# Performance work log

Hardware: AMD Instinct MI355X
Metric: run time of the kernel (lower is better)

The kernel has to match this reference:

```python
import jax, jax.numpy as jnp
import numpy as np

N, E = 50000, 1600000
F_IN, EDGE_DIM, HID, HEADS, NCLS = 64, 16, 128, 4, 40
C = HID // HEADS  # per-head dim = 32


def setup_inputs() -> dict:
    key = jax.random.key(0)
    ks = jax.random.split(key, 20)
    s = 0.1
    inp = {
        'x': jax.random.normal(ks[0], (N, F_IN), jnp.float32),
        'edge_index': jax.random.randint(ks[1], (2, E), 0, N, jnp.int64),
        'edge_attr': jax.random.normal(ks[2], (E, EDGE_DIM), jnp.float32),
        # layer 1 params
        'W1': jax.random.normal(ks[3], (HID, F_IN), jnp.float32) * s,
        'as1': jax.random.normal(ks[4], (HEADS, C), jnp.float32) * s,
        'ad1': jax.random.normal(ks[5], (HEADS, C), jnp.float32) * s,
        'ae1': jax.random.normal(ks[6], (HEADS, C), jnp.float32) * s,
        'We1': jax.random.normal(ks[7], (HID, EDGE_DIM), jnp.float32) * s,
        'b1': jnp.zeros((HID,), jnp.float32),
        # layer 2 params
        'W2': jax.random.normal(ks[8], (HID, HID), jnp.float32) * s,
        'as2': jax.random.normal(ks[9], (HEADS, C), jnp.float32) * s,
        'ad2': jax.random.normal(ks[10], (HEADS, C), jnp.float32) * s,
        'ae2': jax.random.normal(ks[11], (HEADS, C), jnp.float32) * s,
        'We2': jax.random.normal(ks[12], (HID, EDGE_DIM), jnp.float32) * s,
        'b2': jnp.zeros((HID,), jnp.float32),
        # final classifier
        'Wlin': jax.random.normal(ks[13], (NCLS, HID), jnp.float32) * s,
        'blin': jnp.zeros((NCLS,), jnp.float32),
    }
    return inp


def gat_conv(x, src, dst, eattr, W, a_s, a_d, a_e, We, b):
    """PyG GATConv (concat=True, add_self_loops=True, fill_value='mean'), eval mode."""
    n = x.shape[0]
    H, Cd = a_s.shape
    h = (x @ W.T).reshape(n, H, Cd)  # [N,H,C]
    # self-loop edge_attr = per-destination mean of incoming edge_attr
    cnt = jax.ops.segment_sum(jnp.ones((dst.shape[0],), eattr.dtype), dst, num_segments=n)
    mean_ea = jax.ops.segment_sum(eattr, dst, num_segments=n) / jnp.maximum(cnt, 1.0)[:, None]
    loops = jnp.arange(n, dtype=src.dtype)
    s_idx = jnp.concatenate([src, loops])
    d_idx = jnp.concatenate([dst, loops])
    ea = jnp.concatenate([eattr, mean_ea], axis=0)  # [E+N, edge_dim]
    e = (ea @ We.T).reshape(-1, H, Cd)
    # edge-wise attention logits
    alpha = (h * a_s).sum(-1)[s_idx] + (h * a_d).sum(-1)[d_idx] + (e * a_e).sum(-1)  # [E+N,H]
    alpha = jax.nn.leaky_relu(alpha, 0.2)
    # segment softmax over destination neighborhoods (every node has a self-loop)
    amax = jax.ops.segment_max(alpha, d_idx, num_segments=n)
    ex = jnp.exp(alpha - amax[d_idx])
    den = jax.ops.segment_sum(ex, d_idx, num_segments=n)
    coef = ex / (den[d_idx] + 1e-16)
    out = jax.ops.segment_sum(h[s_idx] * coef[:, :, None], d_idx, num_segments=n)
    return out.reshape(n, H * Cd) + b


def reference(x, edge_index, edge_attr, W1, as1, ad1, ae1, We1, b1,
              W2, as2, ad2, ae2, We2, b2, Wlin, blin):
    src, dst = edge_index[0], edge_index[1]
    h = jax.nn.relu(gat_conv(x, src, dst, edge_attr, W1, as1, ad1, ae1, We1, b1))
    h = jax.nn.relu(gat_conv(h, src, dst, edge_attr, W2, as2, ad2, ae2, We2, b2))
    logits = h @ Wlin.T + blin
    return jax.nn.log_softmax(logits, axis=1)
```

## Files before the change

### kernel.cpp

```cpp
#include <hip/hip_runtime.h>
#include <hip/hip_bf16.h>
#include <math.h>


#define CHUNK 2048

typedef __attribute__((ext_vector_type(8))) short short8;
typedef __attribute__((ext_vector_type(4))) float floatx4;
typedef __attribute__((ext_vector_type(2))) float floatx2;

__device__ __forceinline__ unsigned short f2bf(float f) {
  unsigned u = __float_as_uint(f);
  unsigned r = u + 0x7FFFu + ((u >> 16) & 1u);
  return (unsigned short)(r >> 16);
}
__device__ __forceinline__ float bf2f(unsigned short b) {
  return __uint_as_float(((unsigned)b) << 16);
}

__global__ __launch_bounds__(256) void alphaseq_kernel(const float* __restrict__ ea,
                                                       const float* __restrict__ ae1,
                                                       const float* __restrict__ We1,
                                                       const float* __restrict__ ae2,
                                                       const float* __restrict__ We2,
                                                       const int* __restrict__ dst,
                                                       int* __restrict__ bucketCnt,
                                                       uint2* __restrict__ tA1,
                                                       uint2* __restrict__ tA2,
                                                       int E, int NB) {
  __shared__ float wa[128];
  __shared__ int hist[512];
  const int tid = threadIdx.x;
  hist[tid] = 0;
  hist[tid + 256] = 0;
  if (tid < 128) {
    const float* aev = (tid < 64) ? ae1 : ae2;
    const float* Wev = (tid < 64) ? We1 : We2;
    const int h = (tid >> 4) & 3;
    const int d = tid & 15;
    float s = 0.f;
#pragma unroll
    for (int c = 0; c < 32; ++c) s += aev[h * 32 + c] * Wev[(h * 32 + c) * 16 + d];
    wa[tid] = s;
  }
  __syncthreads();
  const int e0 = blockIdx.x * CHUNK, e1 = min(e0 + CHUNK, E);
  for (int e = e0 + tid; e < e1; e += 256) {
    atomicAdd(&hist[dst[e] >> 7], 1);
    const float4* p = (const float4*)(ea + (size_t)e * 16);
    float4 q0 = p[0], q1 = p[1], q2 = p[2], q3 = p[3];
    float v[16] = {q0.x, q0.y, q0.z, q0.w, q1.x, q1.y, q1.z, q1.w,
                   q2.x, q2.y, q2.z, q2.w, q3.x, q3.y, q3.z, q3.w};
    unsigned short rr[8];
#pragma unroll
    for (int h = 0; h < 8; ++h) {
      float s = 0.f;
#pragma unroll
      for (int d = 0; d < 16; ++d) s += v[d] * wa[h * 16 + d];
      rr[h] = f2bf(s);
    }
    uint2 lo, hi;
    lo.x = ((unsigned)rr[1] << 16) | rr[0];
    lo.y = ((unsigned)rr[3] << 16) | rr[2];
    hi.x = ((unsigned)rr[5] << 16) | rr[4];
    hi.y = ((unsigned)rr[7] << 16) | rr[6];
    tA1[e] = lo;
    tA2[e] = hi;
  }
  __syncthreads();
  for (int i = tid; i < NB; i += 256)
    if (hist[i]) atomicAdd(&bucketCnt[i], hist[i]);
}

__global__ __launch_bounds__(512) void scanB_kernel(const int* __restrict__ bucketCnt,
                                                    int* __restrict__ bucketOffs,
                                                    int* __restrict__ bucketPos,
                                                    int* __restrict__ offs,
                                                    int NB, int N, int E) {
  __shared__ int sc[512];
  const int tid = threadIdx.x;
  const int v = (tid < NB) ? bucketCnt[tid] : 0;
  sc[tid] = v;
  __syncthreads();
  for (int off = 1; off < 512; off <<= 1) {
    int t = (tid >= off) ? sc[tid - off] : 0;
    __syncthreads();
    sc[tid] += t;
    __syncthreads();
  }
  const int excl = sc[tid] - v;
  if (tid < NB) { bucketOffs[tid] = excl; bucketPos[tid] = excl; }
  if (tid == 0) { bucketOffs[NB] = E; offs[N] = E; }
}

__global__ __launch_bounds__(512) void partB_kernel(const int* __restrict__ src,
                                                    const int* __restrict__ dst,
                                                    const uint2* __restrict__ tA1,
                                                    const uint2* __restrict__ tA2,
                                                    int* __restrict__ bucketPos,
                                                    int4* __restrict__ binned16,
                                                    int* __restrict__ binned4,
                                                    unsigned char* __restrict__ dlArr,
                                                    int E, int NB) {
  __shared__ int hist[512], gbase[512], lcnt[512];
  const int tid = threadIdx.x;
  const int e0 = blockIdx.x * CHUNK;
  const int e1 = min(e0 + CHUNK, E);
  hist[tid] = 0; lcnt[tid] = 0;
  __syncthreads();
  for (int e = e0 + tid; e < e1; e += 512) atomicAdd(&hist[dst[e] >> 7], 1);
  __syncthreads();
  if (tid < NB && hist[tid] > 0) gbase[tid] = atomicAdd(&bucketPos[tid], hist[tid]);
  __syncthreads();
  for (int e = e0 + tid; e < e1; e += 512) {
    const int d = dst[e];
    const int b = d >> 7;
    const int lr = atomicAdd(&lcnt[b], 1);
    const int g = gbase[b] + lr;
    const uint2 a1 = tA1[e];
    const uint2 a2 = tA2[e];
    int4 v;
    v.x = (src[e] & 0xFFFF) | ((d & 127) << 16);
    v.y = (int)a1.x;
    v.z = (int)a1.y;
    v.w = (int)a2.x;
    binned16[g] = v;
    binned4[g] = (int)a2.y;
    dlArr[g] = (unsigned char)(d & 127);
  }
}

__global__ __launch_bounds__(256) void passC_kernel(const int4* __restrict__ binned16,
                                                    const int* __restrict__ binned4,
                                                    const unsigned char* __restrict__ dlArr,
                                                    const int* __restrict__ bucketOffs,
                                                    int* __restrict__ srcS,
                                                    uint2* __restrict__ aeS1,
                                                    uint2* __restrict__ aeS2,
                                                    int* __restrict__ offs, int N) {
  __shared__ int cnt[128], dbase[129], dpos[128];
  const int tid = threadIdx.x;
  const int b = blockIdx.x;
  const int bo = bucketOffs[b], be = bucketOffs[b + 1];
  const int m = be - bo;
  if (tid < 128) { cnt[tid] = 0; dpos[tid] = 0; }
  __syncthreads();
  for (int t = tid; t < m; t += 256) atomicAdd(&cnt[dlArr[bo + t]], 1);
  __syncthreads();
  for (int off = 1; off < 128; off <<= 1) {
    int t = (tid < 128 && tid >= (unsigned)off) ? cnt[tid - off] : 0;
    __syncthreads();
    if (tid < 128) cnt[tid] += t;
    __syncthreads();
  }
  if (tid == 0) dbase[0] = 0;
  if (tid < 128) dbase[tid + 1] = cnt[tid];
  __syncthreads();
  const int dcnt = min(128, N - (b << 7));
  if (tid < dcnt) offs[(b << 7) + tid] = bo + dbase[tid];
  for (int t = tid; t < m; t += 256) {
    const int4 v = binned16[bo + t];
    const int w4 = binned4[bo + t];
    const int dl = (v.x >> 16) & 127;
    const int p = dbase[dl] + atomicAdd(&dpos[dl], 1);
    srcS[bo + p] = v.x & 0xFFFF;
    aeS1[bo + p] = make_uint2((unsigned)v.y, (unsigned)v.z);
    aeS2[bo + p] = make_uint2((unsigned)v.w, (unsigned)w4);
  }
}

__global__ __launch_bounds__(256) void cvtall_kernel(const float* __restrict__ W1,
                                                     unsigned short* __restrict__ Wb1,
                                                     const float* __restrict__ W2,
                                                     unsigned short* __restrict__ Wb2,
                                                     const float* __restrict__ Wlin,
                                                     unsigned short* __restrict__ whi,
                                                     unsigned short* __restrict__ wlo) {
  const int n1 = 128 * 64, n2 = 128 * 128, n3 = 48 * 128;
  int i = blockIdx.x * 256 + threadIdx.x;
  if (i < n1) {
    Wb1[i] = f2bf(W1[i]);
  } else if (i < n1 + n2) {
    Wb2[i - n1] = f2bf(W2[i - n1]);
  } else if (i < n1 + n2 + n3) {
    const int j = i - n1 - n2;
    float v = (j < 40 * 128) ? Wlin[j] : 0.f;
    unsigned short h = f2bf(v);
    whi[j] = h;
    wlo[j] = f2bf(v - bf2f(h));
  }
}

#define GEMM_SCORE_EPILOGUE()                                                      \
  {                                                                                \
    const float as0 = a_s[ncol0], as1v = a_s[ncol0 + 16];                          \
    const float ad0 = a_d[ncol0], ad1v = a_d[ncol0 + 16];                          \
    _Pragma("unroll") for (int mt = 0; mt < 4; ++mt) {                             \
      _Pragma("unroll") for (int r = 0; r < 4; ++r) {                              \
        float ps = acc[mt][0][r] * as0 + acc[mt][1][r] * as1v;                     \
        float pd = acc[mt][0][r] * ad0 + acc[mt][1][r] * ad1v;                     \
        _Pragma("unroll") for (int off = 8; off; off >>= 1) {                      \
          ps += __shfl_xor(ps, off, 16);                                           \
          pd += __shfl_xor(pd, off, 16);                                           \
        }                                                                          \
        if (l15 == 0) {                                                            \
          const int row = m0 + mt * 16 + (quad << 2) + r;                          \
          if (row < n) {                                                           \
            ssc[(size_t)row * 4 + w] = ps;                                         \
            dsc[(size_t)row * 4 + w] = pd;                                         \
          }                                                                        \
        }                                                                          \
      }                                                                            \
    }                                                                              \
  }

#define GEMM_MFMA_FROM_LDS(KTOT, PA, PB)                                           \
  {                                                                                \
    for (int kc = 0; kc < (KTOT); kc += 32) {                                      \
      const int koff = kc + (quad << 3);                                           \
      short8 a[4], b[2];                                                           \
      _Pragma("unroll") for (int mt = 0; mt < 4; ++mt)                             \
        a[mt] = *(const short8*)(&As[(mt * 16 + l15) * (PA) + koff]);              \
      _Pragma("unroll") for (int nt = 0; nt < 2; ++nt)                             \
        b[nt] = *(const short8*)(&Bs[(ncol0 + nt * 16) * (PB) + koff]);            \
      _Pragma("unroll") for (int mt = 0; mt < 4; ++mt)                             \
        _Pragma("unroll") for (int nt = 0; nt < 2; ++nt)                           \
          acc[mt][nt] =                                                            \
              __builtin_amdgcn_mfma_f32_16x16x32_bf16(a[mt], b[nt], acc[mt][nt],   \
                                                      0, 0, 0);                    \
    }                                                                              \
  }

#define GEMM_WRITE_H()                                                             \
  {                                                                                \
    _Pragma("unroll") for (int mt = 0; mt < 4; ++mt) {                             \
      const int rbase = m0 + mt * 16 + (quad << 2);                                \
      _Pragma("unroll") for (int nt = 0; nt < 2; ++nt) {                           \
        const int col = ncol0 + nt * 16;                                           \
        _Pragma("unroll") for (int r = 0; r < 4; ++r) {                            \
          const int row = rbase + r;                                               \
          if (row < n) H[(size_t)row * 128 + col] = f2bf(acc[mt][nt][r]);          \
        }                                                                          \
      }                                                                            \
    }                                                                              \
  }

__global__ __launch_bounds__(256) void gemm_score_f32_kernel(const float* __restrict__ X,
                                                             const unsigned short* __restrict__ Wb,
                                                             const float* __restrict__ a_s,
                                                             const float* __restrict__ a_d,
                                                             unsigned short* __restrict__ H,
                                                             float* __restrict__ ssc,
                                                             float* __restrict__ dsc,
                                                             int n) {
  __shared__ unsigned short As[64 * 72];
  __shared__ unsigned short Bs[128 * 72];
  const int tid = threadIdx.x;
  const int w = tid >> 6;
  const int lane = tid & 63;
  const int m0 = blockIdx.x * 64;
  const int quad = lane >> 4;
  const int l15 = lane & 15;

#pragma unroll
  for (int it = 0; it < 4; ++it) {
    const int idx = it * 256 + tid;
    const int row = idx >> 4;
    const int c4 = (idx & 15) * 4;
    const int grow = min(m0 + row, n - 1);
    const float4 q = *(const float4*)(X + (size_t)grow * 64 + c4);
    unsigned short* dstp = &As[row * 72 + c4];
    dstp[0] = f2bf(q.x); dstp[1] = f2bf(q.y); dstp[2] = f2bf(q.z); dstp[3] = f2bf(q.w);
  }
#pragma unroll
  for (int it = 0; it < 4; ++it) {
    const int idx = it * 256 + tid;
    const int row = idx >> 3;
    const int c8 = (idx & 7) * 8;
    short8 v = *(const short8*)(Wb + (size_t)row * 64 + c8);
    *(short8*)(&Bs[row * 72 + c8]) = v;
  }
  __syncthreads();

  floatx4 acc[4][2];
#pragma unroll
  for (int mt = 0; mt < 4; ++mt)
#pragma unroll
    for (int nt = 0; nt < 2; ++nt) acc[mt][nt] = (floatx4)(0.f);
  const int ncol0 = (w << 5) + l15;

  GEMM_MFMA_FROM_LDS(64, 72, 72)
  GEMM_WRITE_H()
  GEMM_SCORE_EPILOGUE()
}

__global__ __launch_bounds__(256) void gemm_score_kernel(const unsigned short* __restrict__ X,
                                                         const unsigned short* __restrict__ Wb,
                                                         const float* __restrict__ a_s,
                                                         const float* __restrict__ a_d,
                                                         unsigned short* __restrict__ H,
                                                         float* __restrict__ ssc,
                                                         float* __restrict__ dsc,
                                                         int n) {
  __shared__ unsigned short As[64 * 136];
  __shared__ unsigned short Bs[128 * 136];
  const int tid = threadIdx.x;
  const int w = tid >> 6;
  const int lane = tid & 63;
  const int m0 = blockIdx.x * 64;
  const int quad = lane >> 4;
  const int l15 = lane & 15;

#pragma unroll
  for (int it = 0; it < 4; ++it) {
    const int idx = it * 256 + tid;
    const int row = idx >> 4;
    const int c8 = (idx & 15) * 8;
    const int grow = min(m0 + row, n - 1);
    short8 v = *(const short8*)(X + (size_t)grow * 128 + c8);
    *(short8*)(&As[row * 136 + c8]) = v;
  }
#pragma unroll
  for (int it = 0; it < 8; ++it) {
    const int idx = it * 256 + tid;
    const int row = idx >> 4;
    const int c8 = (idx & 15) * 8;
    short8 v = *(const short8*)(Wb + (size_t)row * 128 + c8);
    *(short8*)(&Bs[row * 136 + c8]) = v;
  }
  __syncthreads();

  floatx4 acc[4][2];
#pragma unroll
  for (int mt = 0; mt < 4; ++mt)
#pragma unroll
    for (int nt = 0; nt < 2; ++nt) acc[mt][nt] = (floatx4)(0.f);
  const int ncol0 = (w << 5) + l15;

  GEMM_MFMA_FROM_LDS(128, 136, 136)
  GEMM_WRITE_H()
  GEMM_SCORE_EPILOGUE()
}

__device__ __forceinline__ float leaky02(float a) { return a > 0.f ? a : 0.2f * a; }
__device__ __forceinline__ float sel4(float4 v, int h) {
  return (h == 0) ? v.x : (h == 1) ? v.y : (h == 2) ? v.z : v.w;
}

__global__ __launch_bounds__(256) void agg_kernel(const unsigned short* __restrict__ hin,
                                                  const float* __restrict__ ssc,
                                                  const float* __restrict__ dsc,
                                                  const unsigned short* __restrict__ aeS,
                                                  const int* __restrict__ offs,
                                                  const int* __restrict__ srcS,
                                                  const float* __restrict__ bias,
                                                  unsigned short* __restrict__ hout, int n) {
  __shared__ int sbuf[4][64];
  __shared__ float pbuf[4][256];
  const int tid = threadIdx.x;
  const int wv = tid >> 6;
  const int lane = tid & 63;
  const int node = blockIdx.x * 4 + wv;
  if (node >= n) return;
  const int l32 = lane & 31;
  const int half = lane >> 5;
  const int ch4 = l32 * 4;
  const int headB = l32 >> 3;
  const float4 dv = *(const float4*)(dsc + (size_t)node * 4);
  float4 l4 = make_float4(0.f, 0.f, 0.f, 0.f);
  float4 sa = make_float4(0.f, 0.f, 0.f, 0.f);
  floatx2 acc01 = (floatx2)(0.f);
  floatx2 acc23 = (floatx2)(0.f);
  const int j0 = offs[node], j1 = offs[node + 1];

  for (int jc = j0; jc < j1; jc += 64) {
    const int len = min(64, j1 - jc);
    float4 p4 = make_float4(0.f, 0.f, 0.f, 0.f);
    int sv = 0;
    if (lane < len) {
      const int j = jc + lane;
      sv = srcS[j];
      const ushort4 aq = *(const ushort4*)(aeS + (size_t)j * 4);
      const float4 ae4 = make_float4(bf2f(aq.x), bf2f(aq.y), bf2f(aq.z), bf2f(aq.w));
      const float4 ss4 = *(const float4*)(ssc + (size_t)sv * 4);
      sa.x += ae4.x; sa.y += ae4.y; sa.z += ae4.z; sa.w += ae4.w;
      p4.x = __expf(leaky02(ss4.x + dv.x + ae4.x));
      p4.y = __expf(leaky02(ss4.y + dv.y + ae4.y));
      p4.z = __expf(leaky02(ss4.z + dv.z + ae4.z));
      p4.w = __expf(leaky02(ss4.w + dv.w + ae4.w));
    }
    sbuf[wv][lane] = sv;
    *(float4*)(&pbuf[wv][lane * 4]) = p4;
    l4.x += p4.x; l4.y += p4.y; l4.z += p4.z; l4.w += p4.w;
    int k = 0;
    for (; k + 8 <= len; k += 8) {
      int s[4];
      float p[4];
      uint2 d[4];
#pragma unroll
      for (int u = 0; u < 4; ++u) {
        const int kk = k + 2 * u + half;
        s[u] = sbuf[wv][kk];
        p[u] = pbuf[wv][kk * 4 + headB];
      }
#pragma unroll
      for (int u = 0; u < 4; ++u)
        d[u] = *(const uint2*)(hin + (size_t)s[u] * 128 + ch4);
#pragma unroll
      for (int u = 0; u < 4; ++u) {
        floatx2 p2; p2.x = p[u]; p2.y = p[u];
        floatx2 h01, h23;
        h01.x = __uint_as_float(d[u].x << 16);
        h01.y = __uint_as_float(d[u].x & 0xFFFF0000u);
        h23.x = __uint_as_float(d[u].y << 16);
        h23.y = __uint_as_float(d[u].y & 0xFFFF0000u);
        acc01 += p2 * h01;
        acc23 += p2 * h23;
      }
    }
    for (; k < len; k += 2) {
      int kk = k + half;
      if (kk < len) {
        int s = sbuf[wv][kk];
        float p = pbuf[wv][kk * 4 + headB];
        uint2 d = *(const uint2*)(hin + (size_t)s * 128 + ch4);
        floatx2 p2; p2.x = p; p2.y = p;
        floatx2 h01, h23;
        h01.x = __uint_as_float(d.x << 16);
        h01.y = __uint_as_float(d.x & 0xFFFF0000u);
        h23.x = __uint_as_float(d.y << 16);
        h23.y = __uint_as_float(d.y & 0xFFFF0000u);
        acc01 += p2 * h01;
        acc23 += p2 * h23;
      }
    }
  }

  float acc[4] = {acc01.x, acc01.y, acc23.x, acc23.y};
#pragma unroll
  for (int off = 32; off; off >>= 1) {
    sa.x += __shfl_xor(sa.x, off);
    sa.y += __shfl_xor(sa.y, off);
    sa.z += __shfl_xor(sa.z, off);
    sa.w += __shfl_xor(sa.w, off);
    l4.x += __shfl_xor(l4.x, off);
    l4.y += __shfl_xor(l4.y, off);
    l4.z += __shfl_xor(l4.z, off);
    l4.w += __shfl_xor(l4.w, off);
  }
#pragma unroll
  for (int i = 0; i < 4; ++i) acc[i] += __shfl_xor(acc[i], 32);

  const int deg = j1 - j0;
  const float invd = 1.f / fmaxf((float)deg, 1.f);
  const float ssn = ssc[(size_t)node * 4 + headB];
  const float aloop = leaky02(ssn + sel4(dv, headB) + sel4(sa, headB) * invd);
  const float pl = __expf(aloop);
  const float lF = sel4(l4, headB) + pl;
  const uint2 hd = *(const uint2*)(hin + (size_t)node * 128 + ch4);
  const float hv0 = __uint_as_float(hd.x << 16);
  const float hv1 = __uint_as_float(hd.x & 0xFFFF0000u);
  const float hv2 = __uint_as_float(hd.y << 16);
  const float hv3 = __uint_as_float(hd.y & 0xFFFF0000u);
  const float inv = 1.f / (lF + 1e-16f);
  const float4 bi = *(const float4*)(bias + ch4);
  const float o0 = fmaxf((acc[0] + pl * hv0) * inv + bi.x, 0.f);
  const float o1 = fmaxf((acc[1] + pl * hv1) * inv + bi.y, 0.f);
  const float o2 = fmaxf((acc[2] + pl * hv2) * inv + bi.z, 0.f);
  const float o3 = fmaxf((acc[3] + pl * hv3) * inv + bi.w, 0.f);
  if (half == 0) {
    ushort4 o;
    o.x = f2bf(o0); o.y = f2bf(o1); o.z = f2bf(o2); o.w = f2bf(o3);
    *(ushort4*)(hout + (size_t)node * 128 + ch4) = o;
  }
}

__global__ __launch_bounds__(256) void classifier_kernel(const unsigned short* __restrict__ h,
                                                         const unsigned short* __restrict__ Whi,
                                                         const unsigned short* __restrict__ Wlo,
                                                         const float* __restrict__ blin,
                                                         float* __restrict__ out, int n) {
  const int w = threadIdx.x >> 6;
  const int lane = threadIdx.x & 63;
  const int quad = lane >> 4;
  const int l15 = lane & 15;
  const int row0 = blockIdx.x * 64 + w * 16;
  if (row0 >= n) return;
  int rowm = row0 + l15;
  if (rowm >= n) rowm = n - 1;
  floatx4 acc[3];
#pragma unroll
  for (int nt = 0; nt < 3; ++nt) acc[nt] = (floatx4)(0.f);
  const size_t hbase = (size_t)rowm * 128;
#pragma unroll
  for (int kc = 0; kc < 128; kc += 32) {
    const int koff = kc + (quad << 3);
    short8 a = *(const short8*)(h + hbase + koff);
#pragma unroll
    for (int nt = 0; nt < 3; ++nt) {
      short8 bh = *(const short8*)(Whi + (size_t)(nt * 16 + l15) * 128 + koff);
      short8 bl = *(const short8*)(Wlo + (size_t)(nt * 16 + l15) * 128 + koff);
      acc[nt] = __builtin_amdgcn_mfma_f32_16x16x32_bf16(a, bh, acc[nt], 0, 0, 0);
      acc[nt] = __builtin_amdgcn_mfma_f32_16x16x32_bf16(a, bl, acc[nt], 0, 0, 0);
    }
  }
  const float bl0 = blin[l15];
  const float bl1 = blin[16 + l15];
  const float bl2 = (l15 < 8) ? blin[32 + l15] : 0.f;
#pragma unroll
  for (int r = 0; r < 4; ++r) {
    const int rrow = row0 + (quad << 2) + r;
    const float v0 = acc[0][r] + bl0;
    const float v1 = acc[1][r] + bl1;
    const float v2 = (l15 < 8) ? (acc[2][r] + bl2) : -INFINITY;
    float m = fmaxf(v0, fmaxf(v1, v2));
#pragma unroll
    for (int off = 8; off; off >>= 1) m = fmaxf(m, __shfl_xor(m, off, 16));
    const float e2 = (l15 < 8) ? __expf(v2 - m) : 0.f;
    float s = __expf(v0 - m) + __expf(v1 - m) + e2;
#pragma unroll
    for (int off = 8; off; off >>= 1) s += __shfl_xor(s, off, 16);
    const float ls = m + __logf(s);
    if (rrow < n) {
      float* po = out + (size_t)rrow * 40;
      po[l15] = v0 - ls;
      po[16 + l15] = v1 - ls;
      if (l15 < 8) po[32 + l15] = v2 - ls;
    }
  }
}

extern "C" void kernel_launch(void* const* d_in, const int* in_sizes, int n_in,
                              void* d_out, int out_size, void* d_ws, size_t ws_size,
                              hipStream_t stream) {
  const float* x    = (const float*)d_in[0];
  const int*   eidx = (const int*)d_in[1];
  const float* ea   = (const float*)d_in[2];
  const float* W1   = (const float*)d_in[3];
  const float* as1  = (const float*)d_in[4];
  const float* ad1  = (const float*)d_in[5];
  const float* ae1w = (const float*)d_in[6];
  const float* We1  = (const float*)d_in[7];
  const float* b1   = (const float*)d_in[8];
  const float* W2   = (const float*)d_in[9];
  const float* as2  = (const float*)d_in[10];
  const float* ad2  = (const float*)d_in[11];
  const float* ae2w = (const float*)d_in[12];
  const float* We2  = (const float*)d_in[13];
  const float* b2   = (const float*)d_in[14];
  const float* Wlin = (const float*)d_in[15];
  const float* blin = (const float*)d_in[16];
  float* out = (float*)d_out;

  const int N = in_sizes[0] / 64;
  const int E = in_sizes[1] / 2;
  const int* src = eidx;
  const int* dst = eidx + E;
  const int NB = (N + 127) >> 7;

  char* wsb = (char*)d_ws;
  size_t off = 0;
  auto alloc = [&](size_t bytes) -> void* {
    void* p = wsb + off;
    off = (off + bytes + 255) & ~(size_t)255;
    return p;
  };
  int* bucketCnt  = (int*)alloc(512 * 4);
  int* bucketOffs = (int*)alloc(513 * 4);
  int* bucketPos  = (int*)alloc(512 * 4);
  int* offs       = (int*)alloc((size_t)(N + 1) * 4);
  uint2* tA1      = (uint2*)alloc((size_t)E * 8);
  uint2* tA2      = (uint2*)alloc((size_t)E * 8);
  void* regC      = alloc((size_t)E * 16);
  int4* binned16  = (int4*)regC;
  unsigned short* hA = (unsigned short*)regC;
  int* binned4    = (int*)alloc((size_t)E * 4);
  unsigned char* dlArr = (unsigned char*)alloc((size_t)E);
  int* srcS       = (int*)alloc((size_t)E * 4);
  unsigned short* Wb1 = (unsigned short*)alloc(128 * 64 * 2);
  unsigned short* Wb2 = (unsigned short*)alloc(128 * 128 * 2);
  unsigned short* Wlh = (unsigned short*)alloc(48 * 128 * 2);
  unsigned short* Wll = (unsigned short*)alloc(48 * 128 * 2);
  float* ssc      = (float*)alloc((size_t)N * 4 * 4);
  float* dsc      = (float*)alloc((size_t)N * 4 * 4);
  unsigned short* hB = (unsigned short*)alloc((size_t)N * 128 * 2);
  uint2* aeS1 = tA1;
  uint2* aeS2 = tA2;

  const int gg = (N + 63) / 64;
  const int gs = (N + 3) / 4;
  const int gp = (E + CHUNK - 1) / CHUNK;
  const int ncvt = 128 * 64 + 128 * 128 + 48 * 128;

  hipMemsetAsync(bucketCnt, 0, 512 * 4, stream);
  alphaseq_kernel<<<gp, 256, 0, stream>>>(ea, ae1w, We1, ae2w, We2, dst, bucketCnt,
                                          tA1, tA2, E, NB);
  scanB_kernel<<<1, 512, 0, stream>>>(bucketCnt, bucketOffs, bucketPos, offs, NB, N, E);
  partB_kernel<<<gp, 512, 0, stream>>>(src, dst, tA1, tA2, bucketPos, binned16, binned4,
                                       dlArr, E, NB);
  passC_kernel<<<NB, 256, 0, stream>>>(binned16, binned4, dlArr, bucketOffs, srcS,
                                       aeS1, aeS2, offs, N);

  cvtall_kernel<<<(ncvt + 255) / 256, 256, 0, stream>>>(W1, Wb1, W2, Wb2, Wlin, Wlh, Wll);

  gemm_score_f32_kernel<<<gg, 256, 0, stream>>>(x, Wb1, as1, ad1, hA, ssc, dsc, N);
  agg_kernel<<<gs, 256, 0, stream>>>(hA, ssc, dsc, (const unsigned short*)aeS1, offs, srcS, b1, hB, N);

  gemm_score_kernel<<<gg, 256, 0, stream>>>(hB, Wb2, as2, ad2, hA, ssc, dsc, N);
  agg_kernel<<<gs, 256, 0, stream>>>(hA, ssc, dsc, (const unsigned short*)aeS2, offs, srcS, b2, hB, N);

  classifier_kernel<<<gg, 256, 0, stream>>>(hB, Wlh, Wll, blin, out, N);
}
```

Before: 491.6 us.

## Fuse edge-attr projection into partition, stage scatter in LDS, swap GEMM operands

The per-edge attention projection of edge_attr moves out of the histogram kernel and into the partition kernel, so the tA1/tA2 intermediate arrays (16 bytes per edge) are no longer written and read back. The partition kernel now builds a local prefix scan and stages records in LDS sorted by bucket, then writes them out contiguously per bucket for more coalesced global stores. The GEMM kernels swap MFMA operand roles so each lane holds four consecutive channels, which allows vectorized ushort4 stores of H and a cheaper score reduction. In exchange the partition kernel uses far more LDS (about 45KB per block, which may lower occupancy), and it adds a binary search per output element.

```diff
diff --git a/kernel.cpp b/kernel.cpp
--- a/kernel.cpp
+++ b/kernel.cpp
@@ -18,58 +18,17 @@
   return __uint_as_float(((unsigned)b) << 16);
 }
 
-__global__ __launch_bounds__(256) void alphaseq_kernel(const float* __restrict__ ea,
-                                                       const float* __restrict__ ae1,
-                                                       const float* __restrict__ We1,
-                                                       const float* __restrict__ ae2,
-                                                       const float* __restrict__ We2,
-                                                       const int* __restrict__ dst,
-                                                       int* __restrict__ bucketCnt,
-                                                       uint2* __restrict__ tA1,
-                                                       uint2* __restrict__ tA2,
-                                                       int E, int NB) {
-  __shared__ float wa[128];
+__global__ __launch_bounds__(512) void hist_kernel(const int* __restrict__ dst,
+                                                   int* __restrict__ bucketCnt,
+                                                   int E, int NB) {
   __shared__ int hist[512];
   const int tid = threadIdx.x;
   hist[tid] = 0;
-  hist[tid + 256] = 0;
-  if (tid < 128) {
-    const float* aev = (tid < 64) ? ae1 : ae2;
-    const float* Wev = (tid < 64) ? We1 : We2;
-    const int h = (tid >> 4) & 3;
-    const int d = tid & 15;
-    float s = 0.f;
-#pragma unroll
-    for (int c = 0; c < 32; ++c) s += aev[h * 32 + c] * Wev[(h * 32 + c) * 16 + d];
-    wa[tid] = s;
-  }
   __syncthreads();
   const int e0 = blockIdx.x * CHUNK, e1 = min(e0 + CHUNK, E);
-  for (int e = e0 + tid; e < e1; e += 256) {
-    atomicAdd(&hist[dst[e] >> 7], 1);
-    const float4* p = (const float4*)(ea + (size_t)e * 16);
-    float4 q0 = p[0], q1 = p[1], q2 = p[2], q3 = p[3];
-    float v[16] = {q0.x, q0.y, q0.z, q0.w, q1.x, q1.y, q1.z, q1.w,
-                   q2.x, q2.y, q2.z, q2.w, q3.x, q3.y, q3.z, q3.w};
-    unsigned short rr[8];
-#pragma unroll
-    for (int h = 0; h < 8; ++h) {
-      float s = 0.f;
-#pragma unroll
-      for (int d = 0; d < 16; ++d) s += v[d] * wa[h * 16 + d];
-      rr[h] = f2bf(s);
-    }
-    uint2 lo, hi;
-    lo.x = ((unsigned)rr[1] << 16) | rr[0];
-    lo.y = ((unsigned)rr[3] << 16) | rr[2];
-    hi.x = ((unsigned)rr[5] << 16) | rr[4];
-    hi.y = ((unsigned)rr[7] << 16) | rr[6];
-    tA1[e] = lo;
-    tA2[e] = hi;
-  }
-  __syncthreads();
-  for (int i = tid; i < NB; i += 256)
-    if (hist[i]) atomicAdd(&bucketCnt[i], hist[i]);
+  for (int e = e0 + tid; e < e1; e += 512) atomicAdd(&hist[dst[e] >> 7], 1);
+  __syncthreads();
+  if (tid < NB && hist[tid]) atomicAdd(&bucketCnt[tid], hist[tid]);
 }
 
 __global__ __launch_bounds__(512) void scanB_kernel(const int* __restrict__ bucketCnt,
@@ -95,38 +54,88 @@
 
 __global__ __launch_bounds__(512) void partB_kernel(const int* __restrict__ src,
                                                     const int* __restrict__ dst,
-                                                    const uint2* __restrict__ tA1,
-                                                    const uint2* __restrict__ tA2,
+                                                    const float* __restrict__ ea,
+                                                    const float* __restrict__ ae1,
+                                                    const float* __restrict__ We1,
+                                                    const float* __restrict__ ae2,
+                                                    const float* __restrict__ We2,
                                                     int* __restrict__ bucketPos,
                                                     int4* __restrict__ binned16,
                                                     int* __restrict__ binned4,
                                                     unsigned char* __restrict__ dlArr,
                                                     int E, int NB) {
-  __shared__ int hist[512], gbase[512], lcnt[512];
+  __shared__ float wa[128];
+  __shared__ int hist[512], sc[512], lbase[513], gbase[512], lcnt[512];
+  __shared__ int4 stg16[CHUNK];
+  __shared__ int stg4[CHUNK];
+  __shared__ unsigned char stg1[CHUNK];
   const int tid = threadIdx.x;
   const int e0 = blockIdx.x * CHUNK;
   const int e1 = min(e0 + CHUNK, E);
   hist[tid] = 0; lcnt[tid] = 0;
+  if (tid < 128) {
+    const float* aev = (tid < 64) ? ae1 : ae2;
+    const float* Wev = (tid < 64) ? We1 : We2;
+    const int h = (tid >> 4) & 3;
+    const int d = tid & 15;
+    float s = 0.f;
+#pragma unroll
+    for (int c = 0; c < 32; ++c) s += aev[h * 32 + c] * Wev[(h * 32 + c) * 16 + d];
+    wa[tid] = s;
+  }
   __syncthreads();
   for (int e = e0 + tid; e < e1; e += 512) atomicAdd(&hist[dst[e] >> 7], 1);
   __syncthreads();
+  sc[tid] = hist[tid];
+  __syncthreads();
+  for (int off = 1; off < 512; off <<= 1) {
+    int t = (tid >= off) ? sc[tid - off] : 0;
+    __syncthreads();
+    sc[tid] += t;
+    __syncthreads();
+  }
+  lbase[tid + 1] = sc[tid];
+  if (tid == 0) lbase[0] = 0;
   if (tid < NB && hist[tid] > 0) gbase[tid] = atomicAdd(&bucketPos[tid], hist[tid]);
   __syncthreads();
   for (int e = e0 + tid; e < e1; e += 512) {
     const int d = dst[e];
     const int b = d >> 7;
     const int lr = atomicAdd(&lcnt[b], 1);
-    const int g = gbase[b] + lr;
-    const uint2 a1 = tA1[e];
-    const uint2 a2 = tA2[e];
+    const float4* p = (const float4*)(ea + (size_t)e * 16);
+    float4 q0 = p[0], q1 = p[1], q2 = p[2], q3 = p[3];
+    float v16[16] = {q0.x, q0.y, q0.z, q0.w, q1.x, q1.y, q1.z, q1.w,
+                     q2.x, q2.y, q2.z, q2.w, q3.x, q3.y, q3.z, q3.w};
+    unsigned short rr[8];
+#pragma unroll
+    for (int h = 0; h < 8; ++h) {
+      float s = 0.f;
+#pragma unroll
+      for (int d2 = 0; d2 < 16; ++d2) s += v16[d2] * wa[h * 16 + d2];
+      rr[h] = f2bf(s);
+    }
     int4 v;
     v.x = (src[e] & 0xFFFF) | ((d & 127) << 16);
-    v.y = (int)a1.x;
-    v.z = (int)a1.y;
-    v.w = (int)a2.x;
-    binned16[g] = v;
-    binned4[g] = (int)a2.y;
-    dlArr[g] = (unsigned char)(d & 127);
+    v.y = (int)(((unsigned)rr[1] << 16) | rr[0]);
+    v.z = (int)(((unsigned)rr[3] << 16) | rr[2]);
+    v.w = (int)(((unsigned)rr[5] << 16) | rr[4]);
+    const int sp = lbase[b] + lr;
+    stg16[sp] = v;
+    stg4[sp] = (int)(((unsigned)rr[7] << 16) | rr[6]);
+    stg1[sp] = (unsigned char)(d & 127);
+  }
+  __syncthreads();
+  const int total = e1 - e0;
+  for (int t = tid; t < total; t += 512) {
+    int lo = 0, hi = 511;
+    while (lo < hi) {
+      int mid = (lo + hi + 1) >> 1;
+      if (lbase[mid] <= t) lo = mid; else hi = mid - 1;
+    }
+    const int g = gbase[lo] + (t - lbase[lo]);
+    binned16[g] = stg16[t];
+    binned4[g] = stg4[t];
+    dlArr[g] = stg1[t];
   }
 }
 
@@ -191,55 +200,61 @@
   }
 }
 
-#define GEMM_SCORE_EPILOGUE()                                                      \
+#define GEMM_MFMA_SWAPPED(KTOT, PA, PB)                                            \
   {                                                                                \
-    const float as0 = a_s[ncol0], as1v = a_s[ncol0 + 16];                          \
-    const float ad0 = a_d[ncol0], ad1v = a_d[ncol0 + 16];                          \
-    _Pragma("unroll") for (int mt = 0; mt < 4; ++mt) {                             \
-      _Pragma("unroll") for (int r = 0; r < 4; ++r) {                              \
-        float ps = acc[mt][0][r] * as0 + acc[mt][1][r] * as1v;                     \
-        float pd = acc[mt][0][r] * ad0 + acc[mt][1][r] * ad1v;                     \
-        _Pragma("unroll") for (int off = 8; off; off >>= 1) {                      \
-          ps += __shfl_xor(ps, off, 16);                                           \
-          pd += __shfl_xor(pd, off, 16);                                           \
-        }                                                                          \
-        if (l15 == 0) {                                                            \
-          const int row = m0 + mt * 16 + (quad << 2) + r;                          \
-          if (row < n) {                                                           \
-            ssc[(size_t)row * 4 + w] = ps;                                         \
-            dsc[(size_t)row * 4 + w] = pd;                                         \
-          }                                                                        \
+    for (int kc = 0; kc < (KTOT); kc += 32) {                                      \
+      const int koff = kc + (quad << 3);                                           \
+      short8 aw[2], bx[4];                                                         \
+      _Pragma("unroll") for (int ct = 0; ct < 2; ++ct)                             \
+        aw[ct] = *(const short8*)(&Bs[(w * 32 + ct * 16 + l15) * (PB) + koff]);    \
+      _Pragma("unroll") for (int nt_ = 0; nt_ < 4; ++nt_)                          \
+        bx[nt_] = *(const short8*)(&As[(nt_ * 16 + l15) * (PA) + koff]);           \
+      _Pragma("unroll") for (int ct = 0; ct < 2; ++ct)                             \
+        _Pragma("unroll") for (int nt_ = 0; nt_ < 4; ++nt_)                        \
+          acc[ct][nt_] =                                                           \
+              __builtin_amdgcn_mfma_f32_16x16x32_bf16(aw[ct], bx[nt_],             \
+                                                      acc[ct][nt_], 0, 0, 0);      \
+    }                                                                              \
+  }
+
+#define GEMM_WRITE_H_SWAPPED()                                                     \
+  {                                                                                \
+    _Pragma("unroll") for (int nt_ = 0; nt_ < 4; ++nt_) {                          \
+      const int node = m0 + nt_ * 16 + l15;                                        \
+      if (node < n) {                                                              \
+        _Pragma("unroll") for (int ct = 0; ct < 2; ++ct) {                         \
+          const int ch = w * 32 + ct * 16 + (quad << 2);                           \
+          ushort4 o;                                                               \
+          o.x = f2bf(acc[ct][nt_][0]); o.y = f2bf(acc[ct][nt_][1]);                \
+          o.z = f2bf(acc[ct][nt_][2]); o.w = f2bf(acc[ct][nt_][3]);                \
+          *(ushort4*)(H + (size_t)node * 128 + ch) = o;                            \
         }                                                                          \
       }                                                                            \
     }                                                                              \
   }
 
-#define GEMM_MFMA_FROM_LDS(KTOT, PA, PB)                                           \
+#define GEMM_SCORE_SWAPPED()                                                       \
   {                                                                                \
-    for (int kc = 0; kc < (KTOT); kc += 32) {                                      \
-      const int koff = kc + (quad << 3);                                           \
-      short8 a[4], b[2];                                                           \
-      _Pragma("unroll") for (int mt = 0; mt < 4; ++mt)                             \
-        a[mt] = *(const short8*)(&As[(mt * 16 + l15) * (PA) + koff]);              \
-      _Pragma("unroll") for (int nt = 0; nt < 2; ++nt)                             \
-        b[nt] = *(const short8*)(&Bs[(ncol0 + nt * 16) * (PB) + koff]);            \
-      _Pragma("unroll") for (int mt = 0; mt < 4; ++mt)                             \
-        _Pragma("unroll") for (int nt = 0; nt < 2; ++nt)                           \
-          acc[mt][nt] =                                                            \
-              __builtin_amdgcn_mfma_f32_16x16x32_bf16(a[mt], b[nt], acc[mt][nt],   \
-                                                      0, 0, 0);                    \
-    }                                                                              \
-  }
-
-#define GEMM_WRITE_H()                                                             \
-  {                                                                                \
-    _Pragma("unroll") for (int mt = 0; mt < 4; ++mt) {                             \
-      const int rbase = m0 + mt * 16 + (quad << 2);                                \
-      _Pragma("unroll") for (int nt = 0; nt < 2; ++nt) {                           \
-        const int col = ncol0 + nt * 16;                                           \
+    float asv[2][4], adv[2][4];                                                    \
+    _Pragma("unroll") for (int ct = 0; ct < 2; ++ct)                               \
+      _Pragma("unroll") for (int r = 0; r < 4; ++r) {                              \
+        const int c = w * 32 + ct * 16 + (quad << 2) + r;                          \
+        asv[ct][r] = a_s[c]; adv[ct][r] = a_d[c];                                  \
+      }                                                                            \
+    _Pragma("unroll") for (int nt_ = 0; nt_ < 4; ++nt_) {                          \
+      float ps = 0.f, pd = 0.f;                                                    \
+      _Pragma("unroll") for (int ct = 0; ct < 2; ++ct)                             \
         _Pragma("unroll") for (int r = 0; r < 4; ++r) {                            \
-          const int row = rbase + r;                                               \
-          if (row < n) H[(size_t)row * 128 + col] = f2bf(acc[mt][nt][r]);          \
+          ps += acc[ct][nt_][r] * asv[ct][r];                                      \
+          pd += acc[ct][nt_][r] * adv[ct][r];                                      \
+        }                                                                          \
+      ps += __shfl_xor(ps, 16); ps += __shfl_xor(ps, 32);                          \
+      pd += __shfl_xor(pd, 16); pd += __shfl_xor(pd, 32);                          \
+      if (lane < 16) {                                                             \
+        const int node = m0 + nt_ * 16 + lane;                                     \
+        if (node < n) {                                                            \
+          ssc[(size_t)node * 4 + w] = ps;                                          \
+          dsc[(size_t)node * 4 + w] = pd;                                          \
         }                                                                          \
       }                                                                            \
     }                                                                              \
@@ -282,16 +297,15 @@
   }
   __syncthreads();
 
-  floatx4 acc[4][2];
-#pragma unroll
-  for (int mt = 0; mt < 4; ++mt)
-#pragma unroll
-    for (int nt = 0; nt < 2; ++nt) acc[mt][nt] = (floatx4)(0.f);
-  const int ncol0 = (w << 5) + l15;
-
-  GEMM_MFMA_FROM_LDS(64, 72, 72)
-  GEMM_WRITE_H()
-  GEMM_SCORE_EPILOGUE()
+  floatx4 acc[2][4];
+#pragma unroll
+  for (int ct = 0; ct < 2; ++ct)
+#pragma unroll
+    for (int nt_ = 0; nt_ < 4; ++nt_) acc[ct][nt_] = (floatx4)(0.f);
+
+  GEMM_MFMA_SWAPPED(64, 72, 72)
+  GEMM_WRITE_H_SWAPPED()
+  GEMM_SCORE_SWAPPED()
 }
 
 __global__ __launch_bounds__(256) void gemm_score_kernel(const unsigned short* __restrict__ X,
@@ -330,16 +344,15 @@
   }
   __syncthreads();
 
-  floatx4 acc[4][2];
-#pragma unroll
-  for (int mt = 0; mt < 4; ++mt)
-#pragma unroll
-    for (int nt = 0; nt < 2; ++nt) acc[mt][nt] = (floatx4)(0.f);
-  const int ncol0 = (w << 5) + l15;
-
-  GEMM_MFMA_FROM_LDS(128, 136, 136)
-  GEMM_WRITE_H()
-  GEMM_SCORE_EPILOGUE()
+  floatx4 acc[2][4];
+#pragma unroll
+  for (int ct = 0; ct < 2; ++ct)
+#pragma unroll
+    for (int nt_ = 0; nt_ < 4; ++nt_) acc[ct][nt_] = (floatx4)(0.f);
+
+  GEMM_MFMA_SWAPPED(128, 136, 136)
+  GEMM_WRITE_H_SWAPPED()
+  GEMM_SCORE_SWAPPED()
 }
 
 __device__ __forceinline__ float leaky02(float a) { return a > 0.f ? a : 0.2f * a; }
@@ -569,8 +582,8 @@
   int* bucketOffs = (int*)alloc(513 * 4);
   int* bucketPos  = (int*)alloc(512 * 4);
   int* offs       = (int*)alloc((size_t)(N + 1) * 4);
-  uint2* tA1      = (uint2*)alloc((size_t)E * 8);
-  uint2* tA2      = (uint2*)alloc((size_t)E * 8);
+  uint2* aeS1     = (uint2*)alloc((size_t)E * 8);
+  uint2* aeS2     = (uint2*)alloc((size_t)E * 8);
   void* regC      = alloc((size_t)E * 16);
   int4* binned16  = (int4*)regC;
   unsigned short* hA = (unsigned short*)regC;
@@ -584,8 +597,6 @@
   float* ssc      = (float*)alloc((size_t)N * 4 * 4);
   float* dsc      = (float*)alloc((size_t)N * 4 * 4);
   unsigned short* hB = (unsigned short*)alloc((size_t)N * 128 * 2);
-  uint2* aeS1 = tA1;
-  uint2* aeS2 = tA2;
 
   const int gg = (N + 63) / 64;
   const int gs = (N + 3) / 4;
@@ -593,11 +604,10 @@
   const int ncvt = 128 * 64 + 128 * 128 + 48 * 128;
 
   hipMemsetAsync(bucketCnt, 0, 512 * 4, stream);
-  alphaseq_kernel<<<gp, 256, 0, stream>>>(ea, ae1w, We1, ae2w, We2, dst, bucketCnt,
-                                          tA1, tA2, E, NB);
+  hist_kernel<<<gp, 512, 0, stream>>>(dst, bucketCnt, E, NB);
   scanB_kernel<<<1, 512, 0, stream>>>(bucketCnt, bucketOffs, bucketPos, offs, NB, N, E);
-  partB_kernel<<<gp, 512, 0, stream>>>(src, dst, tA1, tA2, bucketPos, binned16, binned4,
-                                       dlArr, E, NB);
+  partB_kernel<<<gp, 512, 0, stream>>>(src, dst, ea, ae1w, We1, ae2w, We2, bucketPos,
+                                       binned16, binned4, dlArr, E, NB);
   passC_kernel<<<NB, 256, 0, stream>>>(binned16, binned4, dlArr, bucketOffs, srcS,
                                        aeS1, aeS2, offs, N);
 
```

Result: faster. 464.6 us (-5.5%).
